# Kernel tuning notes

Hardware: AMD Instinct MI355X
Metric: run time of the kernel (lower is better)

## Reference

```python
import jax, jax.numpy as jnp
import numpy as np

TEMPERATURE = 0.05


def setup_inputs() -> dict:
    key = jax.random.key(0)
    k1, k2 = jax.random.split(key)
    B, D = 4096, 1024
    # scale 0.1 keeps pairwise distances O(3) so the original exp(-d/T) is sane
    text_embeddings = 0.1 * jax.random.normal(k1, (B, D), dtype=jnp.float32)
    image_embeddings = 0.1 * jax.random.normal(k2, (B, D), dtype=jnp.float32)
    positive_pairs = jnp.arange(B, dtype=jnp.int32)  # unused by the loss body
    return {
        "text_embeddings": text_embeddings,
        "image_embeddings": image_embeddings,
        "positive_pairs": positive_pairs,
    }


def _pairwise_l2(t, m):
    # ||t_i - m_j|| via GEMM expansion; [B, B]
    sq = (
        jnp.sum(t * t, axis=1, keepdims=True)
        + jnp.sum(m * m, axis=1)[None, :]
        - 2.0 * (t @ m.T)
    )
    return jnp.sqrt(jnp.maximum(sq, 0.0))


def reference(text_embeddings, image_embeddings, positive_pairs):
    # loss_i = -log( exp(-d_ii/T) / sum_{j != i} exp(-d_ij/T) )
    #        = logsumexp_{j != i}(-d_ij/T) + d_ii/T   (exact same math, stable)
    dist = _pairwise_l2(text_embeddings, image_embeddings)  # [B, B]
    logits = -dist / TEMPERATURE
    diag = jnp.diagonal(logits)  # log numerator per row
    B = logits.shape[0]
    eye = jnp.eye(B, dtype=bool)
    masked = jnp.where(eye, -jnp.inf, logits)  # exclude self-term from denom
    lse = jax.nn.logsumexp(masked, axis=1)
    return jnp.mean(lse - diag)
```

## Files before the change

### kernel.cpp

```cpp
#include <hip/hip_runtime.h>
#include <math.h>


#define NB 4096
#define ND 1024
#define LSE_BIAS 90.0f
#define A2 28.85390082f
#define C2 129.8425537f
#define LN2 0.6931471805599453f
#define SCALE1 0x7F7F7F7Fu

typedef int v8i __attribute__((ext_vector_type(8)));
typedef int int4v __attribute__((ext_vector_type(4)));
typedef float v16f __attribute__((ext_vector_type(16)));

__device__ inline void gload_lds16(const unsigned char* g, unsigned char* l) {
  __builtin_amdgcn_global_load_lds(
      (const __attribute__((address_space(1))) unsigned int*)g,
      (__attribute__((address_space(3))) unsigned int*)l, 16, 0, 0);
}

__global__ void prep_kernel(const float* __restrict__ T, const float* __restrict__ M,
                            unsigned char* __restrict__ t8, unsigned char* __restrict__ m8,
                            float* __restrict__ tn, float* __restrict__ mn,
                            float* __restrict__ out) {
  int row = blockIdx.x;
  if (row == 0 && threadIdx.x == 0) out[0] = 0.0f;
  const float* src;
  unsigned char* dst;
  float* nout;
  int r;
  if (row < NB) { src = T; dst = t8; nout = tn; r = row; }
  else          { src = M; dst = m8; nout = mn; r = row - NB; }
  float4 v = ((const float4*)(src + (size_t)r * ND))[threadIdx.x];
  float s = v.x * v.x + v.y * v.y + v.z * v.z + v.w * v.w;
  int p = __builtin_amdgcn_cvt_pk_fp8_f32(v.x, v.y, 0, false);
  p = __builtin_amdgcn_cvt_pk_fp8_f32(v.z, v.w, p, true);
  ((int*)(dst + (size_t)r * ND))[threadIdx.x] = p;
  for (int off = 32; off; off >>= 1) s += __shfl_xor(s, off);
  __shared__ float wsum[4];
  if ((threadIdx.x & 63) == 0) wsum[threadIdx.x >> 6] = s;
  __syncthreads();
  if (threadIdx.x == 0) nout[r] = wsum[0] + wsum[1] + wsum[2] + wsum[3];
}

__launch_bounds__(256, 3)
__global__ void gemm_lse_kernel(const unsigned char* __restrict__ t8,
                                const unsigned char* __restrict__ m8,
                                const float* __restrict__ tn, const float* __restrict__ mn,
                                float* __restrict__ part_s, float* __restrict__ diag) {
  __shared__ unsigned char Al[128 * 128];
  __shared__ unsigned char Bl[128 * 128];
  int rt = blockIdx.x, ct = blockIdx.y;
  int tid = threadIdx.x;
  int wave = tid >> 6, lane = tid & 63;
  int hb = lane >> 5, l31 = lane & 31;

  v16f acc[2][2] = {};

  int l3 = lane >> 3;
  int gc = (lane & 7) ^ l3;
  const unsigned char* gA = t8 + (size_t)(rt * 128 + wave * 32 + l3) * ND + gc * 16;
  const unsigned char* gB = m8 + (size_t)(ct * 128 + wave * 32 + l3) * ND + gc * 16;
  unsigned char* lA = Al + wave * 4096;
  unsigned char* lB = Bl + wave * 4096;

  int wr0 = (wave >> 1) * 64, wc0 = (wave & 1) * 64;
  int sw = l31 & 7;
  int abase = (wr0 + l31) * 128;
  int bbase = (wc0 + l31) * 128;

#pragma unroll 1
  for (int kt = 0; kt < ND / 128; ++kt) {
#pragma unroll
    for (int i = 0; i < 4; ++i) {
      gload_lds16(gA + (size_t)i * 8 * ND, lA + i * 1024);
      gload_lds16(gB + (size_t)i * 8 * ND, lB + i * 1024);
    }
    __syncthreads();
#pragma unroll
    for (int ks = 0; ks < 2; ++ks) {
      int q16 = ((ks * 4 + 2 * hb) ^ sw) * 16;
      int4v a00 = *(const int4v*)&Al[abase + q16];
      int4v a01 = *(const int4v*)&Al[abase + (q16 ^ 16)];
      int4v a10 = *(const int4v*)&Al[abase + 4096 + q16];
      int4v a11 = *(const int4v*)&Al[abase + 4096 + (q16 ^ 16)];
      v8i af0 = (v8i){a00.x, a00.y, a00.z, a00.w, a01.x, a01.y, a01.z, a01.w};
      v8i af1 = (v8i){a10.x, a10.y, a10.z, a10.w, a11.x, a11.y, a11.z, a11.w};
#pragma unroll
      for (int fc = 0; fc < 2; ++fc) {
        int4v b0 = *(const int4v*)&Bl[bbase + fc * 4096 + q16];
        int4v b1 = *(const int4v*)&Bl[bbase + fc * 4096 + (q16 ^ 16)];
        v8i bf = (v8i){b0.x, b0.y, b0.z, b0.w, b1.x, b1.y, b1.z, b1.w};
        acc[0][fc] = __builtin_amdgcn_mfma_scale_f32_32x32x64_f8f6f4(
            af0, bf, acc[0][fc], 0, 0, 0, SCALE1, 0, SCALE1);
        acc[1][fc] = __builtin_amdgcn_mfma_scale_f32_32x32x64_f8f6f4(
            af1, bf, acc[1][fc], 0, 0, 0, SCALE1, 0, SCALE1);
      }
    }
    __syncthreads();
    gA += 128;
    gB += 128;
  }

  int chunk = ct * 2 + (wave & 1);
  bool diagblk = (rt == ct);
  float mnv[2];
#pragma unroll
  for (int fc = 0; fc < 2; ++fc) mnv[fc] = mn[ct * 128 + wc0 + fc * 32 + l31];
#pragma unroll
  for (int fr = 0; fr < 2; ++fr) {
#pragma unroll
    for (int reg = 0; reg < 16; ++reg) {
      int row = (reg & 3) + 8 * (reg >> 2) + 4 * hb;
      int grow = rt * 128 + wr0 + fr * 32 + row;
      float tnr = tn[grow];
      float s = 0.0f;
#pragma unroll
      for (int fc = 0; fc < 2; ++fc) {
        float sq = fmaxf(fmaf(-2.0f, acc[fr][fc][reg], tnr + mnv[fc]), 0.0f);
        float dr = __builtin_amdgcn_sqrtf(sq);
        float e = __builtin_amdgcn_exp2f(fmaf(dr, -A2, C2));
        if (diagblk) {
          int gcol = ct * 128 + wc0 + fc * 32 + l31;
          if (grow == gcol) {
            diag[grow] = -20.0f * dr;
            e = 0.0f;
          }
        }
        s += e;
      }
      for (int m = 16; m; m >>= 1) s += __shfl_xor(s, m);
      if (l31 == 0) part_s[(size_t)grow * 64 + chunk] = s;
    }
  }
}

__global__ void combine_kernel(const float* __restrict__ part_s,
                               const float* __restrict__ diag, float* __restrict__ out) {
  int row = blockIdx.x * 256 + threadIdx.x;
  const float* ps = part_s + (size_t)row * 64;
  float S = 0.0f;
#pragma unroll 8
  for (int c = 0; c < 64; ++c) S += ps[c];
  float loss = (LN2 * __builtin_amdgcn_logf(S) - LSE_BIAS) - diag[row];
  for (int off = 32; off; off >>= 1) loss += __shfl_xor(loss, off);
  __shared__ float wsum[4];
  if ((threadIdx.x & 63) == 0) wsum[threadIdx.x >> 6] = loss;
  __syncthreads();
  if (threadIdx.x == 0)
    atomicAdd(out, (wsum[0] + wsum[1] + wsum[2] + wsum[3]) * (1.0f / (float)NB));
}

extern "C" void kernel_launch(void* const* d_in, const int* in_sizes, int n_in,
                              void* d_out, int out_size, void* d_ws, size_t ws_size,
                              hipStream_t stream) {
  const float* T = (const float*)d_in[0];
  const float* M = (const float*)d_in[1];
  float* out = (float*)d_out;

  unsigned char* t8 = (unsigned char*)d_ws;
  unsigned char* m8 = t8 + (size_t)NB * ND;
  float* fbase = (float*)(m8 + (size_t)NB * ND);
  float* tn = fbase;
  float* mn = tn + NB;
  float* diag = mn + NB;
  float* part_s = diag + NB;

  prep_kernel<<<2 * NB, 256, 0, stream>>>(T, M, t8, m8, tn, mn, out);
  dim3 grid(NB / 128, NB / 128);
  gemm_lse_kernel<<<grid, 256, 0, stream>>>(t8, m8, tn, mn, part_s, diag);
  combine_kernel<<<NB / 256, 256, 0, stream>>>(part_s, diag, out);
}
```

Before: 108.7 us.

## Double-buffer LDS tiles in the GEMM and atomically accumulate row sums

```diff
diff --git a/kernel.cpp b/kernel.cpp
--- a/kernel.cpp
+++ b/kernel.cpp
@@ -23,9 +23,10 @@
 __global__ void prep_kernel(const float* __restrict__ T, const float* __restrict__ M,
                             unsigned char* __restrict__ t8, unsigned char* __restrict__ m8,
                             float* __restrict__ tn, float* __restrict__ mn,
-                            float* __restrict__ out) {
+                            float* __restrict__ S, float* __restrict__ out) {
   int row = blockIdx.x;
-  if (row == 0 && threadIdx.x == 0) out[0] = 0.0f;
+  if (row < 16) S[row * 256 + threadIdx.x] = 0.0f;
+  if (row == 16 && threadIdx.x == 0) out[0] = 0.0f;
   const float* src;
   unsigned char* dst;
   float* nout;
@@ -44,13 +45,49 @@
   if (threadIdx.x == 0) nout[r] = wsum[0] + wsum[1] + wsum[2] + wsum[3];
 }
 
-__launch_bounds__(256, 3)
+
+__device__ inline void compute_tile(const unsigned char* __restrict__ Ab,
+                                    const unsigned char* __restrict__ Bb,
+                                    int abase, int bbase, int hb, int sw,
+                                    v16f (&acc)[2][2]) {
+#pragma unroll
+  for (int ks = 0; ks < 2; ++ks) {
+    int q16 = ((ks * 4 + 2 * hb) ^ sw) * 16;
+    int4v a00 = *(const int4v*)&Ab[abase + q16];
+    int4v a01 = *(const int4v*)&Ab[abase + (q16 ^ 16)];
+    int4v a10 = *(const int4v*)&Ab[abase + 4096 + q16];
+    int4v a11 = *(const int4v*)&Ab[abase + 4096 + (q16 ^ 16)];
+    v8i af0 = (v8i){a00.x, a00.y, a00.z, a00.w, a01.x, a01.y, a01.z, a01.w};
+    v8i af1 = (v8i){a10.x, a10.y, a10.z, a10.w, a11.x, a11.y, a11.z, a11.w};
+#pragma unroll
+    for (int fc = 0; fc < 2; ++fc) {
+      int4v b0 = *(const int4v*)&Bb[bbase + fc * 4096 + q16];
+      int4v b1 = *(const int4v*)&Bb[bbase + fc * 4096 + (q16 ^ 16)];
+      v8i bf = (v8i){b0.x, b0.y, b0.z, b0.w, b1.x, b1.y, b1.z, b1.w};
+      acc[0][fc] = __builtin_amdgcn_mfma_scale_f32_32x32x64_f8f6f4(
+          af0, bf, acc[0][fc], 0, 0, 0, SCALE1, 0, SCALE1);
+      acc[1][fc] = __builtin_amdgcn_mfma_scale_f32_32x32x64_f8f6f4(
+          af1, bf, acc[1][fc], 0, 0, 0, SCALE1, 0, SCALE1);
+    }
+  }
+}
+
+__device__ inline void stage_tile(const unsigned char* gA, const unsigned char* gB,
+                                  unsigned char* lA, unsigned char* lB) {
+#pragma unroll
+  for (int i = 0; i < 4; ++i) {
+    gload_lds16(gA + (size_t)i * 8 * ND, lA + i * 1024);
+    gload_lds16(gB + (size_t)i * 8 * ND, lB + i * 1024);
+  }
+}
+
+__launch_bounds__(256, 2)
 __global__ void gemm_lse_kernel(const unsigned char* __restrict__ t8,
                                 const unsigned char* __restrict__ m8,
                                 const float* __restrict__ tn, const float* __restrict__ mn,
-                                float* __restrict__ part_s, float* __restrict__ diag) {
-  __shared__ unsigned char Al[128 * 128];
-  __shared__ unsigned char Bl[128 * 128];
+                                float* __restrict__ S, float* __restrict__ diag) {
+  __shared__ unsigned char Al[2][128 * 128];
+  __shared__ unsigned char Bl[2][128 * 128];
   int rt = blockIdx.x, ct = blockIdx.y;
   int tid = threadIdx.x;
   int wave = tid >> 6, lane = tid & 63;
@@ -62,48 +99,28 @@
   int gc = (lane & 7) ^ l3;
   const unsigned char* gA = t8 + (size_t)(rt * 128 + wave * 32 + l3) * ND + gc * 16;
   const unsigned char* gB = m8 + (size_t)(ct * 128 + wave * 32 + l3) * ND + gc * 16;
-  unsigned char* lA = Al + wave * 4096;
-  unsigned char* lB = Bl + wave * 4096;
+  int lw = wave * 4096;
 
   int wr0 = (wave >> 1) * 64, wc0 = (wave & 1) * 64;
   int sw = l31 & 7;
   int abase = (wr0 + l31) * 128;
   int bbase = (wc0 + l31) * 128;
 
+  stage_tile(gA, gB, &Al[0][lw], &Bl[0][lw]);
+  __syncthreads();
+
 #pragma unroll 1
-  for (int kt = 0; kt < ND / 128; ++kt) {
-#pragma unroll
-    for (int i = 0; i < 4; ++i) {
-      gload_lds16(gA + (size_t)i * 8 * ND, lA + i * 1024);
-      gload_lds16(gB + (size_t)i * 8 * ND, lB + i * 1024);
-    }
+  for (int it = 0; it < 4; ++it) {
+    stage_tile(gA + 128, gB + 128, &Al[1][lw], &Bl[1][lw]);
+    compute_tile(Al[0], Bl[0], abase, bbase, hb, sw, acc);
     __syncthreads();
-#pragma unroll
-    for (int ks = 0; ks < 2; ++ks) {
-      int q16 = ((ks * 4 + 2 * hb) ^ sw) * 16;
-      int4v a00 = *(const int4v*)&Al[abase + q16];
-      int4v a01 = *(const int4v*)&Al[abase + (q16 ^ 16)];
-      int4v a10 = *(const int4v*)&Al[abase + 4096 + q16];
-      int4v a11 = *(const int4v*)&Al[abase + 4096 + (q16 ^ 16)];
-      v8i af0 = (v8i){a00.x, a00.y, a00.z, a00.w, a01.x, a01.y, a01.z, a01.w};
-      v8i af1 = (v8i){a10.x, a10.y, a10.z, a10.w, a11.x, a11.y, a11.z, a11.w};
-#pragma unroll
-      for (int fc = 0; fc < 2; ++fc) {
-        int4v b0 = *(const int4v*)&Bl[bbase + fc * 4096 + q16];
-        int4v b1 = *(const int4v*)&Bl[bbase + fc * 4096 + (q16 ^ 16)];
-        v8i bf = (v8i){b0.x, b0.y, b0.z, b0.w, b1.x, b1.y, b1.z, b1.w};
-        acc[0][fc] = __builtin_amdgcn_mfma_scale_f32_32x32x64_f8f6f4(
-            af0, bf, acc[0][fc], 0, 0, 0, SCALE1, 0, SCALE1);
-        acc[1][fc] = __builtin_amdgcn_mfma_scale_f32_32x32x64_f8f6f4(
-            af1, bf, acc[1][fc], 0, 0, 0, SCALE1, 0, SCALE1);
-      }
-    }
+    if (it < 3) stage_tile(gA + 256, gB + 256, &Al[0][lw], &Bl[0][lw]);
+    compute_tile(Al[1], Bl[1], abase, bbase, hb, sw, acc);
     __syncthreads();
-    gA += 128;
-    gB += 128;
+    gA += 256;
+    gB += 256;
   }
 
-  int chunk = ct * 2 + (wave & 1);
   bool diagblk = (rt == ct);
   float mnv[2];
 #pragma unroll
@@ -131,19 +148,15 @@
         s += e;
       }
       for (int m = 16; m; m >>= 1) s += __shfl_xor(s, m);
-      if (l31 == 0) part_s[(size_t)grow * 64 + chunk] = s;
+      if (l31 == 0) atomicAdd(&S[grow], s);
     }
   }
 }
 
-__global__ void combine_kernel(const float* __restrict__ part_s,
-                               const float* __restrict__ diag, float* __restrict__ out) {
+__global__ void combine_kernel(const float* __restrict__ S, const float* __restrict__ diag,
+                               float* __restrict__ out) {
   int row = blockIdx.x * 256 + threadIdx.x;
-  const float* ps = part_s + (size_t)row * 64;
-  float S = 0.0f;
-#pragma unroll 8
-  for (int c = 0; c < 64; ++c) S += ps[c];
-  float loss = (LN2 * __builtin_amdgcn_logf(S) - LSE_BIAS) - diag[row];
+  float loss = (LN2 * __builtin_amdgcn_logf(S[row]) - LSE_BIAS) - diag[row];
   for (int off = 32; off; off >>= 1) loss += __shfl_xor(loss, off);
   __shared__ float wsum[4];
   if ((threadIdx.x & 63) == 0) wsum[threadIdx.x >> 6] = loss;
@@ -165,10 +178,10 @@
   float* tn = fbase;
   float* mn = tn + NB;
   float* diag = mn + NB;
-  float* part_s = diag + NB;
+  float* S = diag + NB;
 
-  prep_kernel<<<2 * NB, 256, 0, stream>>>(T, M, t8, m8, tn, mn, out);
+  prep_kernel<<<2 * NB, 256, 0, stream>>>(T, M, t8, m8, tn, mn, S, out);
   dim3 grid(NB / 128, NB / 128);
-  gemm_lse_kernel<<<grid, 256, 0, stream>>>(t8, m8, tn, mn, part_s, diag);
-  combine_kernel<<<NB / 256, 256, 0, stream>>>(part_s, diag, out);
+  gemm_lse_kernel<<<grid, 256, 0, stream>>>(t8, m8, tn, mn, S, diag);
+  combine_kernel<<<NB / 256, 256, 0, stream>>>(S, diag, out);
 }
```

Measured after the change: 135.4 us. 24.6% more time.
